# Optimization experiments

Measured on AMD Instinct MI355X. Metric: run time of the kernel, lower is better.

## Reference

```python
import jax, jax.numpy as jnp
import numpy as np

D_MODEL = 1024
N_HEADS = 16
D_K = D_MODEL // N_HEADS
WINDOW = 512
ROPE_BASE = 10000.0


def _apply_rope(x):
    # x: [B, H, S, D] ; torchtune-style interleaved-pair RoPE
    S, D = x.shape[2], x.shape[3]
    half = D // 2
    inv_freq = 1.0 / (ROPE_BASE ** (jnp.arange(half, dtype=jnp.float32) / half))
    ang = jnp.arange(S, dtype=jnp.float32)[:, None] * inv_freq[None, :]  # [S, half]
    cos = jnp.cos(ang).astype(x.dtype)  # [S, half]
    sin = jnp.sin(ang).astype(x.dtype)
    x_even = x[..., ::2]   # [B,H,S,half]
    x_odd = x[..., 1::2]
    out_even = x_even * cos - x_odd * sin
    out_odd = x_odd * cos + x_even * sin
    return jnp.stack([out_even, out_odd], axis=-1).reshape(x.shape)


def setup_inputs() -> dict:
    key = jax.random.key(0)
    k1, k2, k3 = jax.random.split(key, 3)
    B, S = 2, 2048
    x = jax.random.normal(k1, (B, S, D_MODEL), dtype=jnp.float32)
    # store weights pre-transposed so y = x @ w (same math as nn.Linear)
    w_qkv = jax.random.normal(k2, (D_MODEL, 3 * D_MODEL), dtype=jnp.float32) * (D_MODEL ** -0.5)
    w_o = jax.random.normal(k3, (D_MODEL, D_MODEL), dtype=jnp.float32) * (D_MODEL ** -0.5)
    return {"x": x, "w_qkv": w_qkv, "w_o": w_o}


def reference(x, w_qkv, w_o):
    B, S, _ = x.shape
    qkv = (x @ w_qkv).reshape(B, S, 3, N_HEADS, D_K)
    qkv = jnp.transpose(qkv, (2, 0, 3, 1, 4))  # [3, B, H, S, Dk]
    q, k, v = qkv[0], qkv[1], qkv[2]
    q = _apply_rope(q)
    k = _apply_rope(k)
    # causal sliding-window mask: token i attends to j in [i - WINDOW, i]
    i = jnp.arange(S)[:, None]
    j = jnp.arange(S)[None, :]
    allowed = (j <= i) & (j >= i - WINDOW)
    bias = jnp.where(allowed, 0.0, -jnp.inf).astype(x.dtype)  # [S, S]
    scores = jnp.einsum('bhqd,bhkd->bhqk', q, k) * (D_K ** -0.5) + bias
    attn = jax.nn.softmax(scores, axis=-1)
    out = jnp.einsum('bhqk,bhkd->bhqd', attn, v)  # [B,H,S,Dk]
    out = jnp.transpose(out, (0, 2, 1, 3)).reshape(B, S, D_MODEL)
    return out @ w_o
```

## Files before the change

kernel.cpp:

```cpp
#include <hip/hip_runtime.h>
#include <hip/hip_bf16.h>
#include <math.h>

typedef __bf16 bhalf;
typedef __bf16 bhalf8 __attribute__((ext_vector_type(8)));
typedef float floatx4 __attribute__((ext_vector_type(4)));
typedef _Float16 fh;
typedef _Float16 half4 __attribute__((ext_vector_type(4)));

#define MFMA_BF16(A, B, C) __builtin_amdgcn_mfma_f32_16x16x32_bf16((A), (B), (C), 0, 0, 0)
#define MFMA_F16_K16(A, B, C) __builtin_amdgcn_mfma_f32_16x16x16f16((A), (B), (C), 0, 0, 0)

__device__ inline unsigned short bfb(float f) {
  union { bhalf h; unsigned short u; } c;
  c.h = (bhalf)f;
  return c.u;
}
__device__ inline unsigned short fhb(float f) {
  union { fh h; unsigned short u; } c;
  c.h = (fh)f;
  return c.u;
}

__device__ inline void gload_lds16(const void* g, void* l) {
  typedef const __attribute__((address_space(1))) unsigned int GU;
  typedef __attribute__((address_space(3))) unsigned int LU;
  __builtin_amdgcn_global_load_lds((GU*)g, (LU*)l, 16, 0, 0);
}

__global__ __launch_bounds__(256) void cvt_x_kernel(const float* __restrict__ in,
                                                    bhalf* __restrict__ out) {
  int i = (blockIdx.x * 256 + threadIdx.x) * 8;
  floatx4 v0 = *(const floatx4*)(in + i);
  floatx4 v1 = *(const floatx4*)(in + i + 4);
  bhalf8 o;
  o[0] = (bhalf)v0[0]; o[1] = (bhalf)v0[1]; o[2] = (bhalf)v0[2]; o[3] = (bhalf)v0[3];
  o[4] = (bhalf)v1[0]; o[5] = (bhalf)v1[1]; o[6] = (bhalf)v1[2]; o[7] = (bhalf)v1[3];
  *(bhalf8*)(out + i) = o;
}

__global__ __launch_bounds__(256) void transpose_w_kernel(const float* __restrict__ wqkv,
                                                          const float* __restrict__ wo,
                                                          bhalf* __restrict__ wqkvT,
                                                          bhalf* __restrict__ woT) {
  __shared__ float tile[32][33];
  const int bx = blockIdx.x;
  const float* in = (bx < 96) ? wqkv : wo;
  bhalf* out = (bx < 96) ? wqkvT : woT;
  const int C = (bx < 96) ? 3072 : 1024;
  const int cx = (bx < 96) ? bx : (bx - 96);
  const int R = 1024;
  int c0 = cx * 32, r0 = blockIdx.y * 32;
  int tx = threadIdx.x & 31, ty = threadIdx.x >> 5;
#pragma unroll
  for (int i = 0; i < 32; i += 8)
    tile[ty + i][tx] = in[(size_t)(r0 + ty + i) * C + c0 + tx];
  __syncthreads();
#pragma unroll
  for (int i = 0; i < 32; i += 8)
    out[(size_t)(c0 + ty + i) * R + r0 + tx] = (bhalf)tile[tx][ty + i];
}

template <int EPI, int TN>
__global__ __launch_bounds__(256, 2) void gemm_bt_kernel(
    const bhalf* __restrict__ A, const bhalf* __restrict__ BT, float* __restrict__ Cout,
    bhalf* __restrict__ qb, bhalf* __restrict__ kb, fh* __restrict__ vb,
    int M, int N, int K) {
  constexpr int NT = TN / 32;
  __shared__ __attribute__((aligned(16))) bhalf As[128 * 64];
  __shared__ __attribute__((aligned(16))) bhalf Bs[TN * 64];
  const int tid = threadIdx.x;
  const int lane = tid & 63;
  const int w = tid >> 6, wr = w >> 1, wc = w & 1;
  const int m0 = blockIdx.y * 128, n0 = blockIdx.x * TN;
  const int l15 = lane & 15, lhi = lane >> 4;

  floatx4 acc[4][NT];
#pragma unroll
  for (int i = 0; i < 4; ++i)
#pragma unroll
    for (int j = 0; j < NT; ++j) acc[i][j] = (floatx4){0.f, 0.f, 0.f, 0.f};

  const int srow16 = lane >> 2;
  const int scg = (lane & 3) ^ ((lane >> 3) & 3);
  const bhalf* aP0 = A + (size_t)(m0 + 32 * w + srow16) * K + scg * 8;
  const bhalf* aP1 = aP0 + (size_t)16 * K;
  const bhalf* bP0 = BT + (size_t)(n0 + ((TN == 128) ? 32 * w : 16 * w) + srow16) * K + scg * 8;
  const bhalf* bP1 = bP0 + (size_t)16 * K;
  bhalf* aL0 = &As[(2 * w) * 512];
  bhalf* aL1 = &As[(2 * w + 1) * 512];
  bhalf* bL0 = (TN == 128) ? &Bs[(2 * w) * 512] : &Bs[w * 512];
  bhalf* bL1 = (TN == 128) ? &Bs[(2 * w + 1) * 512] : nullptr;

  const int fro = (l15 * 4 + (lhi ^ ((l15 >> 1) & 3))) * 8;

  for (int k0 = 0; k0 < K; k0 += 64) {
    __syncthreads();
    gload_lds16(aP0 + k0, aL0);
    gload_lds16(aP1 + k0, aL1);
    gload_lds16(bP0 + k0, bL0);
    if constexpr (TN == 128) gload_lds16(bP1 + k0, bL1);
    gload_lds16(aP0 + k0 + 32, aL0 + 4096);
    gload_lds16(aP1 + k0 + 32, aL1 + 4096);
    gload_lds16(bP0 + k0 + 32, bL0 + TN * 32);
    if constexpr (TN == 128) gload_lds16(bP1 + k0 + 32, bL1 + TN * 32);
    __syncthreads();
#pragma unroll
    for (int kh = 0; kh < 2; ++kh) {
      bhalf8 af[4], bf[NT];
#pragma unroll
      for (int mt = 0; mt < 4; ++mt)
        af[mt] = *(const bhalf8*)&As[kh * 4096 + (wr * 4 + mt) * 512 + fro];
#pragma unroll
      for (int nt = 0; nt < NT; ++nt)
        bf[nt] = *(const bhalf8*)&Bs[kh * TN * 32 + (wc * NT + nt) * 512 + fro];
#pragma unroll
      for (int mt = 0; mt < 4; ++mt)
#pragma unroll
        for (int nt = 0; nt < NT; ++nt)
          acc[mt][nt] = MFMA_BF16(af[mt], bf[nt], acc[mt][nt]);
    }
  }

  if constexpr (EPI == 0) {
#pragma unroll
    for (int mt = 0; mt < 4; ++mt)
#pragma unroll
      for (int nt = 0; nt < NT; ++nt)
#pragma unroll
        for (int r = 0; r < 4; ++r) {
          int mg = m0 + wr * 64 + mt * 16 + lhi * 4 + r;
          int ng = n0 + wc * (TN / 2) + nt * 16 + l15;
          Cout[(size_t)mg * N + ng] = acc[mt][nt][r];
        }
  } else {
    const int sel = n0 >> 10;
    if (sel == 2) {
#pragma unroll
      for (int mt = 0; mt < 4; ++mt) {
        int mg = m0 + wr * 64 + mt * 16 + lhi * 4;
        int b = mg >> 11, s0 = mg & 2047;
#pragma unroll
        for (int nt = 0; nt < NT; ++nt) {
          int ng = n0 + wc * (TN / 2) + nt * 16 + l15;
          int h = (ng & 1023) >> 6, d = ng & 63;
          union { unsigned short u[4]; uint2 v2; } pk;
#pragma unroll
          for (int r = 0; r < 4; ++r) pk.u[r] = fhb(acc[mt][nt][r]);
          *(uint2*)&vb[((size_t)((b << 4) + h) * 64 + d) * 2048 + s0] = pk.v2;
        }
      }
    } else {
      bhalf* dst = sel ? kb : qb;
#pragma unroll
      for (int nt = 0; nt < NT; ++nt) {
        int ng = n0 + wc * (TN / 2) + nt * 16 + l15;
        int h = (ng & 1023) >> 6, d = ng & 63;
        float inv = exp2f((float)(d >> 1) * -0.4152410118609203f);
#pragma unroll
        for (int mt = 0; mt < 4; ++mt) {
          int mg = m0 + wr * 64 + mt * 16 + lhi * 4;
          int b = mg >> 11, s0 = mg & 2047;
#pragma unroll
          for (int r = 0; r < 4; ++r) {
            float val = acc[mt][nt][r];
            float partner = __shfl_xor(val, 1, 64);
            if (!(l15 & 1)) {
              float ang = (float)(s0 + r) * inv;
              float sn = __sinf(ang), cs = __cosf(ang);
              float oe = cs * val - sn * partner;
              float oo = cs * partner + sn * val;
              unsigned int u = bfb(oe) | ((unsigned int)bfb(oo) << 16);
              *(unsigned int*)&dst[((size_t)((b << 4) + h) * 2048 + (s0 + r)) * 64 + d] = u;
            }
          }
        }
      }
    }
  }
}

__global__ __launch_bounds__(256, 2) void attn_kernel(const bhalf* __restrict__ qg,
                                                      const bhalf* __restrict__ kg,
                                                      const fh* __restrict__ vt,
                                                      bhalf* __restrict__ attn_out) {
  __shared__ __attribute__((aligned(16))) bhalf Ks[2][8 * 512];
  __shared__ __attribute__((aligned(16))) fh Vs[2][16 * 256];

  const int bh = blockIdx.x;
  const int qt2 = blockIdx.y;
  const int tid = threadIdx.x, lane = tid & 63, w = tid >> 6;
  const int l15 = lane & 15, quad = lane >> 4;
  const int q0 = qt2 * 128;
  const int qtile0 = qt2 * 2;
  const size_t base = (size_t)bh * 2048 * 64;
  const size_t vbase = (size_t)bh * 64 * 2048;

  bhalf8 qa[2][2];
#pragma unroll
  for (int h = 0; h < 2; ++h) {
    const bhalf* qp = qg + base + (size_t)(q0 + h * 64 + w * 16 + l15) * 64 + quad * 8;
    bhalf8 t0 = *(const bhalf8*)qp;
    bhalf8 t1 = *(const bhalf8*)(qp + 32);
#pragma unroll
    for (int j = 0; j < 8; ++j) {
      qa[h][0][j] = (bhalf)((float)t0[j] * 0.18033688f);
      qa[h][1][j] = (bhalf)((float)t1[j] * 0.18033688f);
    }
  }

  const int kOff = (w * 16 + (lane >> 2)) * 64 + (lane & 3) * 8;
  const int vfb0 = 4 * w + (lane >> 5), vfb1 = 4 * w + 2 + (lane >> 5);
  const int vOff0 = ((vfb0 & 3) * 16 + ((lane & 31) >> 1)) * 2048 + w * 16 + (lane & 1) * 8;
  const int vOff1 = ((vfb1 & 3) * 16 + ((lane & 31) >> 1)) * 2048 + w * 16 + (lane & 1) * 8;

  floatx4 O[2][4];
#pragma unroll
  for (int h = 0; h < 2; ++h)
#pragma unroll
    for (int dt = 0; dt < 4; ++dt) O[h][dt] = (floatx4){0.f, 0.f, 0.f, 0.f};
  float lsum[2] = {0.f, 0.f};

  auto stage = [&](int kt, int buf) {
    const bhalf* kp = kg + base + (size_t)(kt * 64) * 64 + kOff;
    gload_lds16(kp, &Ks[buf][(2 * w) * 512]);
    gload_lds16(kp + 32, &Ks[buf][(2 * w + 1) * 512]);
    const fh* vp = vt + vbase + kt * 64;
    gload_lds16(vp + vOff0, &Vs[buf][(2 * w) * 512]);
    gload_lds16(vp + vOff1, &Vs[buf][(2 * w + 1) * 512]);
  };

  auto proc = [&](int buf, int kt, int h) {
    const int diag = qtile0 + h;
    if (kt > diag || kt < diag - 8) return;
    const int iG = q0 + h * 64 + w * 16 + l15;
    floatx4 sf[4];
#pragma unroll
    for (int nt = 0; nt < 4; ++nt) {
      bhalf8 k0 = *(const bhalf8*)&Ks[buf][(nt * 2) * 512 + (l15 * 4 + quad) * 8];
      bhalf8 k1 = *(const bhalf8*)&Ks[buf][(nt * 2 + 1) * 512 + (l15 * 4 + quad) * 8];
      floatx4 s = (floatx4){0.f, 0.f, 0.f, 0.f};
      s = MFMA_BF16(k0, qa[h][0], s);
      s = MFMA_BF16(k1, qa[h][1], s);
      sf[nt] = s;
    }
    if (kt == diag) {
#pragma unroll
      for (int nt = 0; nt < 4; ++nt) {
        int jb = kt * 64 + nt * 16 + quad * 4;
#pragma unroll
        for (int r = 0; r < 4; ++r)
          if (jb + r > iG) sf[nt][r] = -1e30f;
      }
    } else if (kt == diag - 8) {
#pragma unroll
      for (int nt = 0; nt < 4; ++nt) {
        int jb = kt * 64 + nt * 16 + quad * 4;
#pragma unroll
        for (int r = 0; r < 4; ++r)
          if (jb + r + 512 < iG) sf[nt][r] = -1e30f;
      }
    }
#pragma unroll
    for (int nt = 0; nt < 4; ++nt) {
      half4 pf;
#pragma unroll
      for (int r = 0; r < 4; ++r) {
        float p = exp2f(sf[nt][r]);
        lsum[h] += p;
        pf[r] = (fh)p;
      }
#pragma unroll
      for (int dt = 0; dt < 4; ++dt) {
        half4 vf = *(const half4*)&Vs[buf][(nt * 4 + dt) * 256 + (l15 * 4 + quad) * 4];
        O[h][dt] = MFMA_F16_K16(vf, pf, O[h][dt]);
      }
    }
  };

  int ktstart = qtile0 - 8;
  if (ktstart < 0) ktstart = 0;
  const int ktend = qtile0 + 1;
  for (int kt = ktstart; kt <= ktend; kt += 2) {
    const bool two = (kt + 1 <= ktend);
    __syncthreads();
    stage(kt, 0);
    if (two) stage(kt + 1, 1);
    __syncthreads();
    proc(0, kt, 0);
    proc(0, kt, 1);
    if (two) {
      proc(1, kt + 1, 0);
      proc(1, kt + 1, 1);
    }
  }

  const int b = bh >> 4, hh = bh & 15;
#pragma unroll
  for (int h = 0; h < 2; ++h) {
    float t = lsum[h];
    t += __shfl_xor(t, 16, 64);
    t += __shfl_xor(t, 32, 64);
    const float inv = 1.f / t;
    const int s = q0 + h * 64 + w * 16 + l15;
#pragma unroll
    for (int dt = 0; dt < 4; ++dt) {
      union { unsigned short u[4]; uint2 v2; } pk;
#pragma unroll
      for (int r = 0; r < 4; ++r) pk.u[r] = bfb(O[h][dt][r] * inv);
      *(uint2*)&attn_out[(size_t)(b * 2048 + s) * 1024 + hh * 64 + dt * 16 + quad * 4] = pk.v2;
    }
  }
}

extern "C" void kernel_launch(void* const* d_in, const int* in_sizes, int n_in,
                              void* d_out, int out_size, void* d_ws, size_t ws_size,
                              hipStream_t stream) {
  (void)in_sizes; (void)n_in; (void)out_size; (void)ws_size;
  const float* x = (const float*)d_in[0];
  const float* w_qkv = (const float*)d_in[1];
  const float* w_o = (const float*)d_in[2];
  float* out = (float*)d_out;
  char* ws = (char*)d_ws;

  bhalf* x_bf  = (bhalf*)(ws);
  bhalf* wqkvT = (bhalf*)(ws + ((size_t)8 << 20));
  bhalf* woT   = (bhalf*)(ws + ((size_t)14 << 20));
  bhalf* qb    = (bhalf*)(ws + ((size_t)16 << 20));
  bhalf* kb    = (bhalf*)(ws + ((size_t)24 << 20));
  fh*    vb    = (fh*)(ws + ((size_t)32 << 20));
  bhalf* attn  = (bhalf*)(ws + ((size_t)40 << 20));

  cvt_x_kernel<<<2048, 256, 0, stream>>>(x, x_bf);
  transpose_w_kernel<<<dim3(128, 32), 256, 0, stream>>>(w_qkv, w_o, wqkvT, woT);
  gemm_bt_kernel<1, 128><<<dim3(24, 32), 256, 0, stream>>>(x_bf, wqkvT, nullptr, qb, kb, vb,
                                                           4096, 3072, 1024);
  attn_kernel<<<dim3(32, 16), 256, 0, stream>>>(qb, kb, vb, attn);
  gemm_bt_kernel<0, 64><<<dim3(16, 32), 256, 0, stream>>>(attn, woT, out, nullptr, nullptr,
                                                          nullptr, 4096, 1024, 1024);
}
```

Measured before the change: 162.4 us.

## Double-buffer GEMM LDS tiles, merge prep kernels, raise attention occupancy

The GEMM main loop now keeps two LDS buffers and issues the global-to-LDS loads for the next K tile before computing the current one, so memory latency overlaps with MFMA work. The x conversion and the weight transposes are merged into one prep kernel to save a launch. The attention kernel's launch bound asks for three waves per SIMD instead of two, which may force register spilling. Doubling LDS in the GEMM can cut the number of resident blocks, and there is only one barrier per iteration, so the load into the other buffer relies on that single sync to avoid a race.

Result: slower. 169.4 us (+4.3%).

```diff
diff --git a/kernel.cpp b/kernel.cpp
--- a/kernel.cpp
+++ b/kernel.cpp
@@ -28,29 +28,38 @@
   __builtin_amdgcn_global_load_lds((GU*)g, (LU*)l, 16, 0, 0);
 }
 
-__global__ __launch_bounds__(256) void cvt_x_kernel(const float* __restrict__ in,
-                                                    bhalf* __restrict__ out) {
-  int i = (blockIdx.x * 256 + threadIdx.x) * 8;
-  floatx4 v0 = *(const floatx4*)(in + i);
-  floatx4 v1 = *(const floatx4*)(in + i + 4);
-  bhalf8 o;
-  o[0] = (bhalf)v0[0]; o[1] = (bhalf)v0[1]; o[2] = (bhalf)v0[2]; o[3] = (bhalf)v0[3];
-  o[4] = (bhalf)v1[0]; o[5] = (bhalf)v1[1]; o[6] = (bhalf)v1[2]; o[7] = (bhalf)v1[3];
-  *(bhalf8*)(out + i) = o;
-}
-
-__global__ __launch_bounds__(256) void transpose_w_kernel(const float* __restrict__ wqkv,
-                                                          const float* __restrict__ wo,
-                                                          bhalf* __restrict__ wqkvT,
-                                                          bhalf* __restrict__ woT) {
+__global__ __launch_bounds__(256) void prep_kernel(const float* __restrict__ x,
+                                                   const float* __restrict__ wqkv,
+                                                   const float* __restrict__ wo,
+                                                   bhalf* __restrict__ x_bf,
+                                                   bhalf* __restrict__ wqkvT,
+                                                   bhalf* __restrict__ woT) {
   __shared__ float tile[32][33];
   const int bx = blockIdx.x;
-  const float* in = (bx < 96) ? wqkv : wo;
-  bhalf* out = (bx < 96) ? wqkvT : woT;
-  const int C = (bx < 96) ? 3072 : 1024;
-  const int cx = (bx < 96) ? bx : (bx - 96);
+  if (bx < 2048) {
+    int i = (bx * 256 + threadIdx.x) * 8;
+    floatx4 v0 = *(const floatx4*)(x + i);
+    floatx4 v1 = *(const floatx4*)(x + i + 4);
+    bhalf8 o;
+    o[0] = (bhalf)v0[0]; o[1] = (bhalf)v0[1]; o[2] = (bhalf)v0[2]; o[3] = (bhalf)v0[3];
+    o[4] = (bhalf)v1[0]; o[5] = (bhalf)v1[1]; o[6] = (bhalf)v1[2]; o[7] = (bhalf)v1[3];
+    *(bhalf8*)(x_bf + i) = o;
+    return;
+  }
+  const float* in;
+  bhalf* out;
+  int C, cx, ry;
+  if (bx < 5120) {
+    int idx = bx - 2048;
+    in = wqkv; out = wqkvT; C = 3072;
+    cx = idx % 96; ry = idx / 96;
+  } else {
+    int idx = bx - 5120;
+    in = wo; out = woT; C = 1024;
+    cx = idx & 31; ry = idx >> 5;
+  }
   const int R = 1024;
-  int c0 = cx * 32, r0 = blockIdx.y * 32;
+  int c0 = cx * 32, r0 = ry * 32;
   int tx = threadIdx.x & 31, ty = threadIdx.x >> 5;
 #pragma unroll
   for (int i = 0; i < 32; i += 8)
@@ -67,8 +76,8 @@
     bhalf* __restrict__ qb, bhalf* __restrict__ kb, fh* __restrict__ vb,
     int M, int N, int K) {
   constexpr int NT = TN / 32;
-  __shared__ __attribute__((aligned(16))) bhalf As[128 * 64];
-  __shared__ __attribute__((aligned(16))) bhalf Bs[TN * 64];
+  __shared__ __attribute__((aligned(16))) bhalf As[2][128 * 64];
+  __shared__ __attribute__((aligned(16))) bhalf Bs[2][TN * 64];
   const int tid = threadIdx.x;
   const int lane = tid & 63;
   const int w = tid >> 6, wr = w >> 1, wc = w & 1;
@@ -87,39 +96,49 @@
   const bhalf* aP1 = aP0 + (size_t)16 * K;
   const bhalf* bP0 = BT + (size_t)(n0 + ((TN == 128) ? 32 * w : 16 * w) + srow16) * K + scg * 8;
   const bhalf* bP1 = bP0 + (size_t)16 * K;
-  bhalf* aL0 = &As[(2 * w) * 512];
-  bhalf* aL1 = &As[(2 * w + 1) * 512];
-  bhalf* bL0 = (TN == 128) ? &Bs[(2 * w) * 512] : &Bs[w * 512];
-  bhalf* bL1 = (TN == 128) ? &Bs[(2 * w + 1) * 512] : nullptr;
 
   const int fro = (l15 * 4 + (lhi ^ ((l15 >> 1) & 3))) * 8;
 
+  auto stage = [&](int k0, int s) {
+    gload_lds16(aP0 + k0, &As[s][(2 * w) * 512]);
+    gload_lds16(aP1 + k0, &As[s][(2 * w + 1) * 512]);
+    gload_lds16(aP0 + k0 + 32, &As[s][4096 + (2 * w) * 512]);
+    gload_lds16(aP1 + k0 + 32, &As[s][4096 + (2 * w + 1) * 512]);
+    if constexpr (TN == 128) {
+      gload_lds16(bP0 + k0, &Bs[s][(2 * w) * 512]);
+      gload_lds16(bP1 + k0, &Bs[s][(2 * w + 1) * 512]);
+      gload_lds16(bP0 + k0 + 32, &Bs[s][TN * 32 + (2 * w) * 512]);
+      gload_lds16(bP1 + k0 + 32, &Bs[s][TN * 32 + (2 * w + 1) * 512]);
+    } else {
+      gload_lds16(bP0 + k0, &Bs[s][w * 512]);
+      gload_lds16(bP0 + k0 + 32, &Bs[s][TN * 32 + w * 512]);
+    }
+  };
+  auto compute = [&](int s) {
+#pragma unroll
+    for (int kh = 0; kh < 2; ++kh) {
+      bhalf8 af[4], bf[NT];
+#pragma unroll
+      for (int mt = 0; mt < 4; ++mt)
+        af[mt] = *(const bhalf8*)&As[s][kh * 4096 + (wr * 4 + mt) * 512 + fro];
+#pragma unroll
+      for (int nt = 0; nt < NT; ++nt)
+        bf[nt] = *(const bhalf8*)&Bs[s][kh * TN * 32 + (wc * NT + nt) * 512 + fro];
+#pragma unroll
+      for (int mt = 0; mt < 4; ++mt)
+#pragma unroll
+        for (int nt = 0; nt < NT; ++nt)
+          acc[mt][nt] = MFMA_BF16(af[mt], bf[nt], acc[mt][nt]);
+    }
+  };
+
+  stage(0, 0);
+  int buf = 0;
   for (int k0 = 0; k0 < K; k0 += 64) {
     __syncthreads();
-    gload_lds16(aP0 + k0, aL0);
-    gload_lds16(aP1 + k0, aL1);
-    gload_lds16(bP0 + k0, bL0);
-    if constexpr (TN == 128) gload_lds16(bP1 + k0, bL1);
-    gload_lds16(aP0 + k0 + 32, aL0 + 4096);
-    gload_lds16(aP1 + k0 + 32, aL1 + 4096);
-    gload_lds16(bP0 + k0 + 32, bL0 + TN * 32);
-    if constexpr (TN == 128) gload_lds16(bP1 + k0 + 32, bL1 + TN * 32);
-    __syncthreads();
-#pragma unroll
-    for (int kh = 0; kh < 2; ++kh) {
-      bhalf8 af[4], bf[NT];
-#pragma unroll
-      for (int mt = 0; mt < 4; ++mt)
-        af[mt] = *(const bhalf8*)&As[kh * 4096 + (wr * 4 + mt) * 512 + fro];
-#pragma unroll
-      for (int nt = 0; nt < NT; ++nt)
-        bf[nt] = *(const bhalf8*)&Bs[kh * TN * 32 + (wc * NT + nt) * 512 + fro];
-#pragma unroll
-      for (int mt = 0; mt < 4; ++mt)
-#pragma unroll
-        for (int nt = 0; nt < NT; ++nt)
-          acc[mt][nt] = MFMA_BF16(af[mt], bf[nt], acc[mt][nt]);
-    }
+    if (k0 + 64 < K) stage(k0 + 64, buf ^ 1);
+    compute(buf);
+    buf ^= 1;
   }
 
   if constexpr (EPI == 0) {
@@ -180,7 +199,7 @@
   }
 }
 
-__global__ __launch_bounds__(256, 2) void attn_kernel(const bhalf* __restrict__ qg,
+__global__ __launch_bounds__(256, 3) void attn_kernel(const bhalf* __restrict__ qg,
                                                       const bhalf* __restrict__ kg,
                                                       const fh* __restrict__ vt,
                                                       bhalf* __restrict__ attn_out) {
@@ -331,8 +350,7 @@
   fh*    vb    = (fh*)(ws + ((size_t)32 << 20));
   bhalf* attn  = (bhalf*)(ws + ((size_t)40 << 20));
 
-  cvt_x_kernel<<<2048, 256, 0, stream>>>(x, x_bf);
-  transpose_w_kernel<<<dim3(128, 32), 256, 0, stream>>>(w_qkv, w_o, wqkvT, woT);
+  prep_kernel<<<6144, 256, 0, stream>>>(x, w_qkv, w_o, x_bf, wqkvT, woT);
   gemm_bt_kernel<1, 128><<<dim3(24, 32), 256, 0, stream>>>(x_bf, wqkvT, nullptr, qb, kb, vb,
                                                            4096, 3072, 1024);
   attn_kernel<<<dim3(32, 16), 256, 0, stream>>>(qb, kb, vb, attn);
```

## Merge prep kernels, fold Q scale into RoPE epilogue, raise attn occupancy

Applied to the files above, without the earlier changes.

Merges the x conversion and weight transpose kernels into a single prep launch with a flattened grid, which saves one launch. Moves the softmax scale multiply for Q into the QKV GEMM RoPE epilogue, so the attention kernel loads Q fragments directly without converting them. Raises the attention launch-bounds occupancy hint from 2 to 3 and removes the odd-tile guard in the key loop, which assumes the tile count is always even. These are several independent tweaks that trim small fixed costs. The higher occupancy hint may force register spills.

Result: no change. 160.1 us (-1.4%).

```diff
diff --git a/kernel.cpp b/kernel.cpp
--- a/kernel.cpp
+++ b/kernel.cpp
@@ -28,29 +28,38 @@
   __builtin_amdgcn_global_load_lds((GU*)g, (LU*)l, 16, 0, 0);
 }
 
-__global__ __launch_bounds__(256) void cvt_x_kernel(const float* __restrict__ in,
-                                                    bhalf* __restrict__ out) {
-  int i = (blockIdx.x * 256 + threadIdx.x) * 8;
-  floatx4 v0 = *(const floatx4*)(in + i);
-  floatx4 v1 = *(const floatx4*)(in + i + 4);
-  bhalf8 o;
-  o[0] = (bhalf)v0[0]; o[1] = (bhalf)v0[1]; o[2] = (bhalf)v0[2]; o[3] = (bhalf)v0[3];
-  o[4] = (bhalf)v1[0]; o[5] = (bhalf)v1[1]; o[6] = (bhalf)v1[2]; o[7] = (bhalf)v1[3];
-  *(bhalf8*)(out + i) = o;
-}
-
-__global__ __launch_bounds__(256) void transpose_w_kernel(const float* __restrict__ wqkv,
-                                                          const float* __restrict__ wo,
-                                                          bhalf* __restrict__ wqkvT,
-                                                          bhalf* __restrict__ woT) {
+__global__ __launch_bounds__(256) void prep_kernel(const float* __restrict__ x,
+                                                   const float* __restrict__ wqkv,
+                                                   const float* __restrict__ wo,
+                                                   bhalf* __restrict__ x_bf,
+                                                   bhalf* __restrict__ wqkvT,
+                                                   bhalf* __restrict__ woT) {
   __shared__ float tile[32][33];
   const int bx = blockIdx.x;
-  const float* in = (bx < 96) ? wqkv : wo;
-  bhalf* out = (bx < 96) ? wqkvT : woT;
-  const int C = (bx < 96) ? 3072 : 1024;
-  const int cx = (bx < 96) ? bx : (bx - 96);
+  if (bx < 2048) {
+    int i = (bx * 256 + threadIdx.x) * 8;
+    floatx4 v0 = *(const floatx4*)(x + i);
+    floatx4 v1 = *(const floatx4*)(x + i + 4);
+    bhalf8 o;
+    o[0] = (bhalf)v0[0]; o[1] = (bhalf)v0[1]; o[2] = (bhalf)v0[2]; o[3] = (bhalf)v0[3];
+    o[4] = (bhalf)v1[0]; o[5] = (bhalf)v1[1]; o[6] = (bhalf)v1[2]; o[7] = (bhalf)v1[3];
+    *(bhalf8*)(x_bf + i) = o;
+    return;
+  }
+  const float* in;
+  bhalf* out;
+  int C, cx, ry;
+  if (bx < 5120) {
+    int idx = bx - 2048;
+    in = wqkv; out = wqkvT; C = 3072;
+    cx = idx % 96; ry = idx / 96;
+  } else {
+    int idx = bx - 5120;
+    in = wo; out = woT; C = 1024;
+    cx = idx & 31; ry = idx >> 5;
+  }
   const int R = 1024;
-  int c0 = cx * 32, r0 = blockIdx.y * 32;
+  int c0 = cx * 32, r0 = ry * 32;
   int tx = threadIdx.x & 31, ty = threadIdx.x >> 5;
 #pragma unroll
   for (int i = 0; i < 32; i += 8)
@@ -152,6 +161,7 @@
       }
     } else {
       bhalf* dst = sel ? kb : qb;
+      const float post = sel ? 1.0f : 0.18033688f;
 #pragma unroll
       for (int nt = 0; nt < NT; ++nt) {
         int ng = n0 + wc * (TN / 2) + nt * 16 + l15;
@@ -168,8 +178,8 @@
             if (!(l15 & 1)) {
               float ang = (float)(s0 + r) * inv;
               float sn = __sinf(ang), cs = __cosf(ang);
-              float oe = cs * val - sn * partner;
-              float oo = cs * partner + sn * val;
+              float oe = (cs * val - sn * partner) * post;
+              float oo = (cs * partner + sn * val) * post;
               unsigned int u = bfb(oe) | ((unsigned int)bfb(oo) << 16);
               *(unsigned int*)&dst[((size_t)((b << 4) + h) * 2048 + (s0 + r)) * 64 + d] = u;
             }
@@ -180,7 +190,7 @@
   }
 }
 
-__global__ __launch_bounds__(256, 2) void attn_kernel(const bhalf* __restrict__ qg,
+__global__ __launch_bounds__(256, 3) void attn_kernel(const bhalf* __restrict__ qg,
                                                       const bhalf* __restrict__ kg,
                                                       const fh* __restrict__ vt,
                                                       bhalf* __restrict__ attn_out) {
@@ -200,13 +210,8 @@
 #pragma unroll
   for (int h = 0; h < 2; ++h) {
     const bhalf* qp = qg + base + (size_t)(q0 + h * 64 + w * 16 + l15) * 64 + quad * 8;
-    bhalf8 t0 = *(const bhalf8*)qp;
-    bhalf8 t1 = *(const bhalf8*)(qp + 32);
-#pragma unroll
-    for (int j = 0; j < 8; ++j) {
-      qa[h][0][j] = (bhalf)((float)t0[j] * 0.18033688f);
-      qa[h][1][j] = (bhalf)((float)t1[j] * 0.18033688f);
-    }
+    qa[h][0] = *(const bhalf8*)qp;
+    qa[h][1] = *(const bhalf8*)(qp + 32);
   }
 
   const int kOff = (w * 16 + (lane >> 2)) * 64 + (lane & 3) * 8;
@@ -282,17 +287,14 @@
   if (ktstart < 0) ktstart = 0;
   const int ktend = qtile0 + 1;
   for (int kt = ktstart; kt <= ktend; kt += 2) {
-    const bool two = (kt + 1 <= ktend);
     __syncthreads();
     stage(kt, 0);
-    if (two) stage(kt + 1, 1);
+    stage(kt + 1, 1);
     __syncthreads();
     proc(0, kt, 0);
     proc(0, kt, 1);
-    if (two) {
-      proc(1, kt + 1, 0);
-      proc(1, kt + 1, 1);
-    }
+    proc(1, kt + 1, 0);
+    proc(1, kt + 1, 1);
   }
 
   const int b = bh >> 4, hh = bh & 15;
@@ -331,8 +333,7 @@
   fh*    vb    = (fh*)(ws + ((size_t)32 << 20));
   bhalf* attn  = (bhalf*)(ws + ((size_t)40 << 20));
 
-  cvt_x_kernel<<<2048, 256, 0, stream>>>(x, x_bf);
-  transpose_w_kernel<<<dim3(128, 32), 256, 0, stream>>>(w_qkv, w_o, wqkvT, woT);
+  prep_kernel<<<6144, 256, 0, stream>>>(x, w_qkv, w_o, x_bf, wqkvT, woT);
   gemm_bt_kernel<1, 128><<<dim3(24, 32), 256, 0, stream>>>(x_bf, wqkvT, nullptr, qb, kb, vb,
                                                            4096, 3072, 1024);
   attn_kernel<<<dim3(32, 16), 256, 0, stream>>>(qb, kb, vb, attn);
```
